# Kernel tuning notes

Measured on AMD Instinct MI355X. Metric: run time of the kernel, lower is better.

Reference implementation:

```python
import jax, jax.numpy as jnp
import numpy as np

N_COLS = 107
CAT_SLICES = [(1, 10), (10, 26), (27, 34), (34, 49), (49, 55), (55, 60), (60, 62), (65, 107)]
MSE_COLS = [0, 26, 62, 63, 64]
BATCH = 524288


def setup_inputs() -> dict:
    key = jax.random.key(0)
    k_dec, k_cont, k_cat = jax.random.split(key, 3)
    data_decoded = jax.random.normal(k_dec, (BATCH, N_COLS), dtype=jnp.float32)
    # Build data_true: continuous cols random, categorical slices exactly one-hot.
    data_true = jax.random.uniform(k_cont, (BATCH, N_COLS), dtype=jnp.float32)
    rows = jnp.arange(BATCH)
    for i, (s, e) in enumerate(CAT_SLICES):
        kk = jax.random.fold_in(k_cat, i)
        labels = jax.random.randint(kk, (BATCH,), 0, e - s)
        data_true = data_true.at[:, s:e].set(0.0)
        data_true = data_true.at[rows, s + labels].set(1.0)
    return {"data_decoded": data_decoded, "data_true": data_true, "batch_size": BATCH}


def _ce(logits, onehot_true):
    # torch nonzero()[:,1] on an exact one-hot slice == argmax
    labels = jnp.argmax(onehot_true, axis=1)
    logp = jax.nn.log_softmax(logits, axis=1)
    return -jnp.mean(jnp.take_along_axis(logp, labels[:, None], axis=1))


def _mse(a, b):
    d = a - b
    return jnp.mean(d * d)


def reference(data_decoded, data_true, batch_size):
    mse_loss = jnp.float32(0.0)
    for c in MSE_COLS:
        mse_loss = mse_loss + _mse(data_decoded[:, c], data_true[:, c])
    ce_loss = jnp.float32(0.0)
    for s, e in CAT_SLICES:
        ce_loss = ce_loss + _ce(data_decoded[:, s:e], data_true[:, s:e])
    multi_loss = mse_loss + ce_loss
    return multi_loss, mse_loss, ce_loss
```

## Files before the change

### kernel.cpp

```cpp
#include <hip/hip_runtime.h>
#include <float.h>

#define NCOLS 107
#define THREADS 256
#define BLOCKS 2048

typedef float f4 __attribute__((ext_vector_type(4)));

__device__ __forceinline__ int col_class(int c) {
    if (c == 0 || c == 26 || (c >= 62 && c <= 64)) return -1;
    if (c < 10) return 0;
    if (c < 26) return 1;
    if (c < 34) return 2;
    if (c < 49) return 3;
    if (c < 55) return 4;
    if (c < 60) return 5;
    if (c < 62) return 6;
    return 7;
}

struct RowState {
    float m[8], s[8], mse, dot;
};

__device__ __forceinline__ void proc(int c, float d, float t, RowState& st) {
    int k = col_class(c);
    if (k < 0) {
        float df = d - t;
        st.mse = fmaf(df, df, st.mse);
    } else {
        st.dot = fmaf(d, t, st.dot);
        float mn = fmaxf(st.m[k], d);
        st.s[k] = fmaf(st.s[k], __expf(st.m[k] - mn), __expf(d - mn));
        st.m[k] = mn;
    }
}

__device__ __forceinline__ f4 ld4(const float* p) {
    f4 v;
    __builtin_memcpy(&v, p, 16);
    return v;
}

__global__ __launch_bounds__(THREADS) void multiloss_main(
        const float* __restrict__ dec, const float* __restrict__ tru,
        float2* __restrict__ ws, int nrows) {
    int tid    = blockIdx.x * THREADS + threadIdx.x;
    int stride = gridDim.x * THREADS;

    float mse = 0.0f, dot = 0.0f, lsesum = 0.0f;

    for (int row = tid; row < nrows; row += stride) {
        const float* dr = dec + (size_t)row * NCOLS;
        const float* tr = tru + (size_t)row * NCOLS;
        RowState st;
#pragma unroll
        for (int k = 0; k < 8; ++k) { st.m[k] = -FLT_MAX; st.s[k] = 0.0f; }
        st.mse = 0.0f; st.dot = 0.0f;

#pragma unroll
        for (int g = 0; g < 26; ++g) {
            f4 dv = ld4(dr + 4 * g);
            f4 tv = ld4(tr + 4 * g);
            proc(4 * g + 0, dv.x, tv.x, st);
            proc(4 * g + 1, dv.y, tv.y, st);
            proc(4 * g + 2, dv.z, tv.z, st);
            proc(4 * g + 3, dv.w, tv.w, st);
        }
        {
            f4 dv = ld4(dr + 103);
            f4 tv = ld4(tr + 103);
            proc(104, dv.y, tv.y, st);
            proc(105, dv.z, tv.z, st);
            proc(106, dv.w, tv.w, st);
        }
#pragma unroll
        for (int k = 0; k < 8; ++k) lsesum += st.m[k] + __logf(st.s[k]);
        mse += st.mse;
        dot += st.dot;
    }

    float ce = lsesum - dot;
#pragma unroll
    for (int off = 32; off > 0; off >>= 1) {
        mse += __shfl_down(mse, off, 64);
        ce  += __shfl_down(ce,  off, 64);
    }
    if ((threadIdx.x & 63) == 0)
        ws[tid >> 6] = make_float2(mse, ce);
}

__global__ __launch_bounds__(256) void multiloss_fin(
        const float2* __restrict__ ws, float* __restrict__ out,
        int nslots, float invN) {
    float m = 0.0f, c = 0.0f;
    for (int i = threadIdx.x; i < nslots; i += 256) {
        float2 v = ws[i];
        m += v.x; c += v.y;
    }
#pragma unroll
    for (int off = 32; off > 0; off >>= 1) {
        m += __shfl_down(m, off, 64);
        c += __shfl_down(c, off, 64);
    }
    __shared__ float sm[4], sc[4];
    int wid  = threadIdx.x >> 6;
    int lane = threadIdx.x & 63;
    if (lane == 0) { sm[wid] = m; sc[wid] = c; }
    __syncthreads();
    if (threadIdx.x == 0) {
        float mse = (sm[0] + sm[1] + sm[2] + sm[3]) * invN;
        float ce  = (sc[0] + sc[1] + sc[2] + sc[3]) * invN;
        out[0] = mse + ce;
        out[1] = mse;
        out[2] = ce;
    }
}

extern "C" void kernel_launch(void* const* d_in, const int* in_sizes, int n_in,
                              void* d_out, int out_size, void* d_ws, size_t ws_size,
                              hipStream_t stream) {
    const float* dec = (const float*)d_in[0];
    const float* tru = (const float*)d_in[1];
    int nrows  = in_sizes[0] / NCOLS;
    int nslots = BLOCKS * THREADS / 64;
    float2* ws = (float2*)d_ws;
    multiloss_main<<<BLOCKS, THREADS, 0, stream>>>(dec, tru, ws, nrows);
    multiloss_fin<<<1, 256, 0, stream>>>(ws, (float*)d_out, nslots,
                                         1.0f / (float)nrows);
}
```

Before: 503.7 us.

## Coalesce tile loads through LDS and drop max-subtraction from log-sum-exp

```diff
diff --git a/kernel.cpp b/kernel.cpp
--- a/kernel.cpp
+++ b/kernel.cpp
@@ -1,93 +1,86 @@
 #include <hip/hip_runtime.h>
-#include <float.h>
 
 #define NCOLS 107
+#define ROWS_PER_TILE 16
+#define TILE_FLOATS (ROWS_PER_TILE * NCOLS)
+#define TILE_VEC (TILE_FLOATS / 4)
 #define THREADS 256
+#define WAVES_PER_BLOCK 4
 #define BLOCKS 2048
+#define TILES_PER_WAVE 4
 
 typedef float f4 __attribute__((ext_vector_type(4)));
 
-__device__ __forceinline__ int col_class(int c) {
-    if (c == 0 || c == 26 || (c >= 62 && c <= 64)) return -1;
-    if (c < 10) return 0;
-    if (c < 26) return 1;
-    if (c < 34) return 2;
-    if (c < 49) return 3;
-    if (c < 55) return 4;
-    if (c < 60) return 5;
-    if (c < 62) return 6;
-    return 7;
-}
-
-struct RowState {
-    float m[8], s[8], mse, dot;
-};
-
-__device__ __forceinline__ void proc(int c, float d, float t, RowState& st) {
-    int k = col_class(c);
-    if (k < 0) {
-        float df = d - t;
-        st.mse = fmaf(df, df, st.mse);
-    } else {
-        st.dot = fmaf(d, t, st.dot);
-        float mn = fmaxf(st.m[k], d);
-        st.s[k] = fmaf(st.s[k], __expf(st.m[k] - mn), __expf(d - mn));
-        st.m[k] = mn;
-    }
-}
-
-__device__ __forceinline__ f4 ld4(const float* p) {
-    f4 v;
-    __builtin_memcpy(&v, p, 16);
-    return v;
+template<int S, int E>
+__device__ __forceinline__ float slice_lse(const float* dr) {
+    constexpr int L = E - S;
+    float s = 0.0f;
+#pragma unroll
+    for (int j = 0; j < L; ++j) s += __expf(dr[S + j]);
+    return __logf(s);
 }
 
 __global__ __launch_bounds__(THREADS) void multiloss_main(
         const float* __restrict__ dec, const float* __restrict__ tru,
-        float2* __restrict__ ws, int nrows) {
-    int tid    = blockIdx.x * THREADS + threadIdx.x;
-    int stride = gridDim.x * THREADS;
+        float2* __restrict__ ws, int ntiles) {
+    __shared__ float sdec[WAVES_PER_BLOCK * TILE_FLOATS];
+    int gwave = (blockIdx.x * THREADS + threadIdx.x) >> 6;
+    int lane  = threadIdx.x & 63;
+    float* buf = sdec + (threadIdx.x >> 6) * TILE_FLOATS;
 
-    float mse = 0.0f, dot = 0.0f, lsesum = 0.0f;
+    float mse = 0.0f, dot = 0.0f, lse = 0.0f;
 
-    for (int row = tid; row < nrows; row += stride) {
-        const float* dr = dec + (size_t)row * NCOLS;
-        const float* tr = tru + (size_t)row * NCOLS;
-        RowState st;
-#pragma unroll
-        for (int k = 0; k < 8; ++k) { st.m[k] = -FLT_MAX; st.s[k] = 0.0f; }
-        st.mse = 0.0f; st.dot = 0.0f;
+    for (int t = 0; t < TILES_PER_WAVE; ++t) {
+        int tile = gwave * TILES_PER_WAVE + t;
+        if (tile >= ntiles) break;
+        const f4* gd = (const f4*)(dec + (size_t)tile * TILE_FLOATS);
+        const f4* gt = (const f4*)(tru + (size_t)tile * TILE_FLOATS);
 
 #pragma unroll
-        for (int g = 0; g < 26; ++g) {
-            f4 dv = ld4(dr + 4 * g);
-            f4 tv = ld4(tr + 4 * g);
-            proc(4 * g + 0, dv.x, tv.x, st);
-            proc(4 * g + 1, dv.y, tv.y, st);
-            proc(4 * g + 2, dv.z, tv.z, st);
-            proc(4 * g + 3, dv.w, tv.w, st);
+        for (int i = 0; i < 7; ++i) {
+            int idx = i * 64 + lane;
+            if (idx < TILE_VEC) {
+                f4 dv = gd[idx];
+                f4 tv = gt[idx];
+                ((f4*)buf)[idx] = dv;
+                int col0 = (idx * 4) % NCOLS;
+#pragma unroll
+                for (int k = 0; k < 4; ++k) {
+                    int col = col0 + k;
+                    if (col >= NCOLS) col -= NCOLS;
+                    float d = dv[k], tt = tv[k];
+                    bool ismse = (col == 0) | (col == 26) |
+                                 ((unsigned)(col - 62) <= 2u);
+                    float df = d - tt;
+                    mse += ismse ? df * df : 0.0f;
+                    dot += ismse ? 0.0f : d * tt;
+                }
+            }
         }
-        {
-            f4 dv = ld4(dr + 103);
-            f4 tv = ld4(tr + 103);
-            proc(104, dv.y, tv.y, st);
-            proc(105, dv.z, tv.z, st);
-            proc(106, dv.w, tv.w, st);
+
+        int row  = lane & 15;
+        int part = lane >> 4;
+        const float* dr = buf + row * NCOLS;
+        if (part == 0) {
+            lse += slice_lse<65, 107>(dr);
+        } else if (part == 1) {
+            lse += slice_lse<10, 26>(dr) + slice_lse<34, 49>(dr);
+        } else if (part == 2) {
+            lse += slice_lse<1, 10>(dr) + slice_lse<27, 34>(dr)
+                 + slice_lse<49, 55>(dr);
+        } else {
+            lse += slice_lse<55, 60>(dr) + slice_lse<60, 62>(dr);
         }
-#pragma unroll
-        for (int k = 0; k < 8; ++k) lsesum += st.m[k] + __logf(st.s[k]);
-        mse += st.mse;
-        dot += st.dot;
     }
 
-    float ce = lsesum - dot;
+    float ce = lse - dot;
 #pragma unroll
     for (int off = 32; off > 0; off >>= 1) {
         mse += __shfl_down(mse, off, 64);
         ce  += __shfl_down(ce,  off, 64);
     }
-    if ((threadIdx.x & 63) == 0)
-        ws[tid >> 6] = make_float2(mse, ce);
+    if (lane == 0)
+        ws[gwave] = make_float2(mse, ce);
 }
 
 __global__ __launch_bounds__(256) void multiloss_fin(
@@ -123,9 +116,10 @@
     const float* dec = (const float*)d_in[0];
     const float* tru = (const float*)d_in[1];
     int nrows  = in_sizes[0] / NCOLS;
+    int ntiles = nrows / ROWS_PER_TILE;
     int nslots = BLOCKS * THREADS / 64;
     float2* ws = (float2*)d_ws;
-    multiloss_main<<<BLOCKS, THREADS, 0, stream>>>(dec, tru, ws, nrows);
+    multiloss_main<<<BLOCKS, THREADS, 0, stream>>>(dec, tru, ws, ntiles);
     multiloss_fin<<<1, 256, 0, stream>>>(ws, (float*)d_out, nslots,
                                          1.0f / (float)nrows);
 }
```

Measured after the change: 448.1 us. 1.12x faster.
